# Performance work log

Measured on AMD Instinct MI355X. Metric: run time of the kernel, lower is better.

## Reference

```python
import jax, jax.numpy as jnp
import numpy as np

CHANS = [32, 32, 64, 64, 128, 128]
IN_CHANS = [1, 32, 32, 64, 64, 128]
BETA = 0.25  # VectorQuantizer_reset default; ResidualVQ's beta=0.4 is never forwarded
BN_EPS = 1e-5


def setup_inputs() -> dict:
    key = jax.random.key(0)
    ks = jax.random.split(key, 20)
    B, L, IDIM, H, NE = 64, 2000, 80, 256, 1024
    inp = {"speech": jax.random.normal(ks[0], (B, L, IDIM), jnp.float32)}
    for i, (ci, co) in enumerate(zip(IN_CHANS, CHANS)):
        inp[f"cw{i}"] = jax.random.normal(ks[1 + i], (co, ci, 3, 3), jnp.float32) * 0.05
        inp[f"g{i}"] = jnp.ones((co,), jnp.float32)
        inp[f"b{i}"] = jnp.zeros((co,), jnp.float32)
    inp["w_ih"] = jax.random.normal(ks[10], (3 * H, 256), jnp.float32) * 0.05
    inp["w_hh"] = jax.random.normal(ks[11], (3 * H, H), jnp.float32) * 0.05
    inp["bih"] = jnp.zeros((3 * H,), jnp.float32)
    inp["bhh"] = jnp.zeros((3 * H,), jnp.float32)
    for j, k in zip((1, 2, 3), (12, 13, 14)):
        inp[f"cb{j}"] = jax.random.uniform(ks[k], (NE, H), jnp.float32, -1.0 / NE, 1.0 / NE)
    return inp


def conv_bn_relu(x, w, g, b):
    # Conv2d(k=3, stride=2, pad=1, bias=False) + BatchNorm2d (training-mode batch stats) + ReLU
    y = jax.lax.conv_general_dilated(x, w, (2, 2), [(1, 1), (1, 1)],
                                     dimension_numbers=("NCHW", "OIHW", "NCHW"))
    mu = jnp.mean(y, axis=(0, 2, 3), keepdims=True)
    var = jnp.mean((y - mu) ** 2, axis=(0, 2, 3), keepdims=True)  # biased, as torch BN
    y = (y - mu) * jax.lax.rsqrt(var + BN_EPS) * g.reshape(1, -1, 1, 1) + b.reshape(1, -1, 1, 1)
    return jax.nn.relu(y)


def gru_last_hidden(x, w_ih, w_hh, bih, bhh):
    # x: (B, T, D). PyTorch GRU, 1 layer, h0 = 0; returns last hidden state (B, H).
    B = x.shape[0]
    H = w_hh.shape[1]
    xw = jnp.einsum("btd,gd->btg", x, w_ih) + bih  # (B, T, 3H), precompute input gates

    def step(h, xt):
        gh = h @ w_hh.T + bhh
        i_r, i_z, i_n = jnp.split(xt, 3, axis=-1)
        h_r, h_z, h_n = jnp.split(gh, 3, axis=-1)
        r = jax.nn.sigmoid(i_r + h_r)
        z = jax.nn.sigmoid(i_z + h_z)
        n = jnp.tanh(i_n + r * h_n)
        return (1.0 - z) * n + z * h, None

    h0 = jnp.zeros((B, H), x.dtype)
    hT, _ = jax.lax.scan(step, h0, jnp.swapaxes(xw, 0, 1))
    return hT


def vq(z, E):
    # z: (B, e_dim), E: (n_e, e_dim). Nearest-neighbor quantize + straight-through.
    d = jnp.sum(z * z, axis=1, keepdims=True) + jnp.sum(E * E, axis=1) - 2.0 * (z @ E.T)
    idx = jnp.argmin(d, axis=1)  # (B,)
    z_q = E[idx]
    loss = jnp.mean((jax.lax.stop_gradient(z_q) - z) ** 2) \
         + BETA * jnp.mean((z_q - jax.lax.stop_gradient(z)) ** 2)
    z_q_st = z + jax.lax.stop_gradient(z_q - z)
    return z_q_st, loss, idx


def reference(speech, cw0, g0, b0, cw1, g1, b1, cw2, g2, b2, cw3, g3, b3,
              cw4, g4, b4, cw5, g5, b5, w_ih, w_hh, bih, bhh, cb1, cb2, cb3):
    x = speech[:, None, :, :]  # (B, 1, L, idim)
    for w, g, b in ((cw0, g0, b0), (cw1, g1, b1), (cw2, g2, b2),
                    (cw3, g3, b3), (cw4, g4, b4), (cw5, g5, b5)):
        x = conv_bn_relu(x, w, g, b)
    B, C, T, F = x.shape
    hs = x.transpose(0, 2, 1, 3).reshape(B, T, C * F)  # (B, T', C*F)
    ref_embs = gru_last_hidden(hs, w_ih, w_hh, bih, bhh)  # (B, 256)

    residual = ref_embs
    zq1, l1, i1 = vq(residual, cb1)
    residual = residual - zq1
    zq2, l2, i2 = vq(residual, cb2)
    residual = residual - zq2
    zq3, l3, i3 = vq(residual, cb3)

    z_q_out = jnp.concatenate([zq1, zq2, zq3], axis=1)  # (B, 3*e_dim)
    vq_loss = l1 + l2 + l3
    codebooks = (zq1, zq2, zq3, zq1 + zq2 + zq3)
    return (z_q_out, vq_loss, i1[:, None], codebooks)
```

## Files before the change

### kernel.cpp

```cpp
#include <hip/hip_runtime.h>
#include <math.h>


__global__ __launch_bounds__(256) void prep_kernel(
    const float* __restrict__ w_ih, const float* __restrict__ w_hh,
    const float* __restrict__ cb0, const float* __restrict__ cb1,
    const float* __restrict__ cb2, float* __restrict__ w_ihT,
    float* __restrict__ w_hhT, float* __restrict__ ET, float* __restrict__ sE) {
  int tid = threadIdx.x;
  int y = blockIdx.y;
  if (y < 5) {
    const float* in;
    float* outp;
    int R, C;
    if (y == 0) { in = w_ih; outp = w_ihT; R = 768; C = 256; }
    else if (y == 1) { in = w_hh; outp = w_hhT; R = 768; C = 256; }
    else {
      in = (y == 2 ? cb0 : (y == 3 ? cb1 : cb2));
      outp = ET + (size_t)(y - 2) * 262144;
      R = 1024; C = 256;
    }
    int n = R * C;
    for (int t = blockIdx.x * 256 + tid; t < n; t += 64 * 256) {
      int i = t / C, j = t % C;
      outp[(size_t)j * R + i] = in[t];
    }
  } else {
    int wid = tid >> 6, lane = tid & 63;
    for (int c = blockIdx.x * 4 + wid; c < 3072; c += 64 * 4) {
      const float* E = (c < 1024 ? cb0 : (c < 2048 ? cb1 : cb2));
      int cc = c & 1023;
      float4 v4 = ((const float4*)(E + (size_t)cc * 256))[lane];
      float ssum = v4.x * v4.x + v4.y * v4.y + v4.z * v4.z + v4.w * v4.w;
#pragma unroll
      for (int m = 32; m >= 1; m >>= 1) ssum += __shfl_xor(ssum, m, 64);
      if (lane == 0) sE[c] = ssum;
    }
  }
}

__global__ __launch_bounds__(256) void conv0_stats_kernel(
    const float* __restrict__ speech, const float* __restrict__ w0,
    float* __restrict__ part) {
  constexpr int SPR = 41, SPH = 49;
  __shared__ float spE[SPH * SPR];
  __shared__ float spO[SPH * SPR];
  const int tid = threadIdx.x;
  const int bx = blockIdx.x;
  const int b = blockIdx.z;
  const int to0 = bx * 24;
  const int sr0 = 2 * to0 - 1;
  const float* sb = speech + (size_t)b * 160000;
  for (int i = tid; i < SPH * 81; i += 256) {
    int r = i / 81, c = i % 81;
    int gr = sr0 + r, gc = c - 1;
    float v = (gr >= 0 && gr < 2000 && gc >= 0 && gc < 80) ? sb[gr * 80 + gc] : 0.f;
    float* pl = (c & 1) ? spO : spE;
    pl[r * SPR + (c >> 1)] = v;
  }
  __syncthreads();

  const int fo = tid % 40;
  const int trr = tid / 40;
  const bool rowok = (trr < 6);
  const int r0 = rowok ? trr * 4 : 0;

  float xv4[4][9];
  {
    int e0 = (2 * r0) * SPR + fo;
    float p0 = spE[e0], p1 = spO[e0], p2 = spE[e0 + 1];
#pragma unroll
    for (int k = 0; k < 4; ++k) {
      int mr = (2 * (r0 + k) + 1) * SPR + fo;
      int br = mr + SPR;
      xv4[k][0] = p0; xv4[k][1] = p1; xv4[k][2] = p2;
      xv4[k][3] = spE[mr]; xv4[k][4] = spO[mr]; xv4[k][5] = spE[mr + 1];
      xv4[k][6] = spE[br]; xv4[k][7] = spO[br]; xv4[k][8] = spE[br + 1];
      p0 = xv4[k][6]; p1 = xv4[k][7]; p2 = xv4[k][8];
    }
  }
  bool val[4];
#pragma unroll
  for (int k = 0; k < 4; ++k) val[k] = rowok && (to0 + r0 + k < 1000);

  float s[32], q[32];
#pragma unroll
  for (int c = 0; c < 32; ++c) { s[c] = 0.f; q[c] = 0.f; }
#pragma unroll
  for (int c = 0; c < 32; ++c) {
    const float* wk = w0 + c * 9;
    float w0v = wk[0], w1v = wk[1], w2v = wk[2], w3v = wk[3], w4v = wk[4];
    float w5v = wk[5], w6v = wk[6], w7v = wk[7], w8v = wk[8];
#pragma unroll
    for (int k = 0; k < 4; ++k) {
      float a = xv4[k][0] * w0v;
      a = fmaf(xv4[k][1], w1v, a); a = fmaf(xv4[k][2], w2v, a);
      a = fmaf(xv4[k][3], w3v, a); a = fmaf(xv4[k][4], w4v, a);
      a = fmaf(xv4[k][5], w5v, a); a = fmaf(xv4[k][6], w6v, a);
      a = fmaf(xv4[k][7], w7v, a); a = fmaf(xv4[k][8], w8v, a);
      if (val[k]) { s[c] += a; q[c] = fmaf(a, a, q[c]); }
    }
  }
  const int wid = tid >> 6;
  const int lane = tid & 63;
  const int pidx = ((b * 42 + bx) << 2) | wid;
#pragma unroll
  for (int c = 0; c < 32; ++c) {
    float ss = s[c], qq = q[c];
#pragma unroll
    for (int m = 32; m >= 1; m >>= 1) {
      ss += __shfl_xor(ss, m, 64);
      qq += __shfl_xor(qq, m, 64);
    }
    if (lane == 0) {
      part[(size_t)c * 10752 + pidx] = ss;
      part[(size_t)(32 + c) * 10752 + pidx] = qq;
    }
  }
}

__global__ __launch_bounds__(256) void conv1_fused_kernel(
    const float* __restrict__ speech, const float* __restrict__ w0,
    const float* __restrict__ aff0, const float* __restrict__ w1,
    float* __restrict__ y, float* __restrict__ part) {
  constexpr int SPR = 41, SPH = 51;
  constexpr int LPS = 21, LTH = 25, LPL = LTH * LPS;
  __shared__ float spE[SPH * SPR];
  __shared__ float spO[SPH * SPR];
  __shared__ float l0t[2][2 * LPL];
  const int tid = threadIdx.x;
  const int bx = blockIdx.x;
  const int b = blockIdx.z;
  const int to0 = bx * 12;
  const int l0r0 = 2 * to0 - 1;
  const int sr0 = 4 * to0 - 3;
  const float* sb = speech + (size_t)b * 160000;
  for (int i = tid; i < SPH * 81; i += 256) {
    int r = i / 81, c = i % 81;
    int gr = sr0 + r, gc = c - 1;
    float v = (gr >= 0 && gr < 2000 && gc >= 0 && gc < 80) ? sb[gr * 80 + gc] : 0.f;
    float* pl = (c & 1) ? spO : spE;
    pl[r * SPR + (c >> 1)] = v;
  }

  const int fc = tid % 42;
  const int fr0 = tid / 42;
  const bool filler = (tid < 210);
  const int wcol = fc - 1;
  const bool colok = (wcol >= 0) && (wcol < 40);
  const int wc = colok ? wcol : 0;
  const int r0 = fr0 * 5;
  const int lplane = (fc & 1) * LPL;
  const int lidx = fc >> 1;

  const int fo = tid % 20;
  const int tr = tid / 20;
  const int to = to0 + tr;
  const bool active = (tr < 12) && (to < 500);
  const int trc = (tr < 12) ? tr : 0;

  float acc[32];
#pragma unroll
  for (int c = 0; c < 32; ++c) acc[c] = 0.f;

  __syncthreads();

#define L0FILL(CIDX, BF)                                                      \
  if (filler) {                                                               \
    const float* wk = w0 + (CIDX) * 9;                                        \
    const float wv0 = wk[0], wv1 = wk[1], wv2 = wk[2], wv3 = wk[3];           \
    const float wv4 = wk[4], wv5 = wk[5], wv6 = wk[6], wv7 = wk[7];           \
    const float wv8 = wk[8];                                                  \
    const float sc = aff0[CIDX], sh = aff0[32 + (CIDX)];                      \
    int e0 = (2 * r0) * SPR + wc;                                             \
    float t0 = spE[e0], t1 = spO[e0], t2 = spE[e0 + 1];                       \
    _Pragma("unroll")                                                         \
    for (int k = 0; k < 5; ++k) {                                             \
      int r = r0 + k;                                                         \
      int mr = (2 * r + 1) * SPR + wc;                                        \
      int br = mr + SPR;                                                      \
      float m0 = spE[mr], m1 = spO[mr], m2 = spE[mr + 1];                     \
      float b0 = spE[br], b1 = spO[br], b2 = spE[br + 1];                     \
      float a = t0 * wv0;                                                     \
      a = fmaf(t1, wv1, a); a = fmaf(t2, wv2, a);                             \
      a = fmaf(m0, wv3, a); a = fmaf(m1, wv4, a); a = fmaf(m2, wv5, a);       \
      a = fmaf(b0, wv6, a); a = fmaf(b1, wv7, a); a = fmaf(b2, wv8, a);       \
      int h0 = l0r0 + r;                                                      \
      bool ok = colok && h0 >= 0 && h0 < 1000;                                \
      float vv = ok ? fmaxf(fmaf(a, sc, sh), 0.f) : 0.f;                      \
      l0t[BF][lplane + r * LPS + lidx] = vv;                                  \
      t0 = b0; t1 = b1; t2 = b2;                                              \
    }                                                                         \
  }

  L0FILL(0, 0)
  __syncthreads();

  for (int ci = 0; ci < 32; ++ci) {
    int cur = ci & 1;
    if (ci + 1 < 32) { L0FILL(ci + 1, cur ^ 1) }
    float xv[9];
    const int rb = 2 * trc;
#pragma unroll
    for (int t = 0; t < 9; ++t) {
      int dr = t / 3, m = t % 3;
      xv[t] = l0t[cur][(m == 1 ? LPL : 0) + (rb + dr) * LPS + fo + (m == 2 ? 1 : 0)];
    }
    const float* wp = w1 + ci * 9;
#pragma unroll
    for (int c = 0; c < 32; ++c) {
      const float* wcp = wp + (size_t)c * 32 * 9;
#pragma unroll
      for (int t = 0; t < 9; ++t) acc[c] = fmaf(xv[t], wcp[t], acc[c]);
    }
    __syncthreads();
  }
#undef L0FILL

  if (active) {
#pragma unroll
    for (int c = 0; c < 32; ++c)
      y[(((size_t)b * 32 + c) * 500 + to) * 20 + fo] = acc[c];
  }

  const int wid = tid >> 6;
  const int lane = tid & 63;
  const int pidx = ((b * 42 + bx) << 2) | wid;
#pragma unroll
  for (int c = 0; c < 32; ++c) {
    float v = active ? acc[c] : 0.f;
    float qq = v * v;
#pragma unroll
    for (int m = 32; m >= 1; m >>= 1) {
      v += __shfl_xor(v, m, 64);
      qq += __shfl_xor(qq, m, 64);
    }
    if (lane == 0) {
      part[(size_t)c * 10752 + pidx] = v;
      part[(size_t)(32 + c) * 10752 + pidx] = qq;
    }
  }
}

template <int CI, int COG, int WO, int ROWS, int WI, int HI, int HO>
__global__ __launch_bounds__(256) void conv_kernel(
    const float* __restrict__ x, const float* __restrict__ w,
    const float* __restrict__ aff, float* __restrict__ y, int CO,
    float* __restrict__ part) {
  constexpr int TW = WI + 2;
  constexpr int PE = (TW + 1) / 2;
  constexpr int PS = PE | 1;
  constexpr int TH = 2 * ROWS + 1;
  constexpr int PL = TH * PS;
  constexpr int TN = TH * TW;
  constexpr int F = (TN + 255) / 256;
  __shared__ float tile[2][2 * PL];

  const int tid = threadIdx.x;
  const int fo = tid % WO;
  const int tr = tid / WO;
  const int to0 = blockIdx.x * ROWS;
  const int to = to0 + tr;
  const int co0 = blockIdx.y * COG;
  const int b = blockIdx.z;
  const bool active = (tr < ROWS) && (to < HO);
  const int trc = (tr < ROWS) ? tr : 0;

  int fa[F], fof[F];
  bool fv[F], fw[F];
#pragma unroll
  for (int j = 0; j < F; ++j) {
    int i = tid + j * 256;
    int r = i / TW, c = i % TW;
    int gih = 2 * to0 - 1 + r;
    int giw = c - 1;
    bool inb = (i < TN);
    bool v = inb && gih >= 0 && gih < HI && giw >= 0 && giw < WI;
    fw[j] = inb;
    fv[j] = v;
    fof[j] = v ? (gih * WI + giw) : 0;
    fa[j] = inb ? ((c & 1) * PL + r * PS + (c >> 1)) : 0;
  }

  float acc[COG];
#pragma unroll
  for (int c = 0; c < COG; ++c) acc[c] = 0.f;

  const float* xb = x + (size_t)b * CI * HI * WI;

  {
    const float sc = aff[0], sh = aff[CI];
#pragma unroll
    for (int j = 0; j < F; ++j) {
      if (fw[j]) {
        float v = xb[fof[j]];
        v = fv[j] ? fmaxf(fmaf(v, sc, sh), 0.f) : 0.f;
        tile[0][fa[j]] = v;
      }
    }
  }
  __syncthreads();

  for (int ci = 0; ci < CI; ++ci) {
    int cur = ci & 1;
    if (ci + 1 < CI) {
      const float* xc = xb + (size_t)(ci + 1) * HI * WI;
      const float sc = aff[ci + 1], sh = aff[CI + ci + 1];
#pragma unroll
      for (int j = 0; j < F; ++j) {
        if (fw[j]) {
          float v = xc[fof[j]];
          v = fv[j] ? fmaxf(fmaf(v, sc, sh), 0.f) : 0.f;
          tile[cur ^ 1][fa[j]] = v;
        }
      }
    }
    float xv[9];
    const int rb = 2 * trc;
#pragma unroll
    for (int t = 0; t < 9; ++t) {
      int dr = t / 3, m = t % 3;
      xv[t] = tile[cur][(m == 1 ? PL : 0) + (rb + dr) * PS + fo + (m == 2 ? 1 : 0)];
    }
    const float* wp = w + ((size_t)co0 * CI + ci) * 9;
#pragma unroll
    for (int c = 0; c < COG; ++c) {
      const float* wc = wp + (size_t)c * CI * 9;
#pragma unroll
      for (int t = 0; t < 9; ++t) acc[c] = fmaf(xv[t], wc[t], acc[c]);
    }
    __syncthreads();
  }

  if (active) {
#pragma unroll
    for (int c = 0; c < COG; ++c)
      y[(((size_t)b * CO + co0 + c) * HO + to) * WO + fo] = acc[c];
  }

  const int wid = tid >> 6;
  const int lane = tid & 63;
  const int P = (int)(gridDim.z * gridDim.x) * 4;
  const int pidx = ((b * (int)gridDim.x + (int)blockIdx.x) << 2) | wid;
#pragma unroll
  for (int c = 0; c < COG; ++c) {
    float v = active ? acc[c] : 0.f;
    float qq = v * v;
#pragma unroll
    for (int m = 32; m >= 1; m >>= 1) {
      v += __shfl_xor(v, m, 64);
      qq += __shfl_xor(qq, m, 64);
    }
    if (lane == 0) {
      part[(size_t)(co0 + c) * P + pidx] = v;
      part[(size_t)(CO + co0 + c) * P + pidx] = qq;
    }
  }
}

__global__ __launch_bounds__(256) void conv5_kernel(
    const float* __restrict__ x, const float* __restrict__ w5,
    const float* __restrict__ aff, float* __restrict__ part5) {
  constexpr int TW = 5, PS = 3, TH = 65, PL = TH * PS, TN = TH * TW;
  __shared__ float tile[2][2 * PL];
  const int tid = threadIdx.x;
  const int p = tid & 63;
  const int to = p >> 1, fo = p & 1;
  const int cog = tid >> 6;
  const int co0 = cog * 32;
  const int ci0 = blockIdx.y * 32;
  const int b = blockIdx.z;

  int fa[2], fof[2];
  bool fv[2], fw[2];
#pragma unroll
  for (int j = 0; j < 2; ++j) {
    int i = tid + j * 256;
    int r = i / TW, c = i % TW;
    int gih = r - 1, giw = c - 1;
    bool inb = (i < TN);
    bool v = inb && gih >= 0 && gih < 63 && giw >= 0 && giw < 3;
    fw[j] = inb;
    fv[j] = v;
    fof[j] = v ? (gih * 3 + giw) : 0;
    fa[j] = inb ? ((c & 1) * PL + r * PS + (c >> 1)) : 0;
  }

  float acc[32];
#pragma unroll
  for (int c = 0; c < 32; ++c) acc[c] = 0.f;

  const float* xb = x + (size_t)b * 128 * 189;

  {
    const float sc = aff[ci0], sh = aff[128 + ci0];
    const float* xc = xb + (size_t)ci0 * 189;
#pragma unroll
    for (int j = 0; j < 2; ++j) {
      if (fw[j]) {
        float v = xc[fof[j]];
        v = fv[j] ? fmaxf(fmaf(v, sc, sh), 0.f) : 0.f;
        tile[0][fa[j]] = v;
      }
    }
  }
  __syncthreads();

  for (int cc = 0; cc < 32; ++cc) {
    int cur = cc & 1;
    int ci = ci0 + cc;
    if (cc + 1 < 32) {
      const float* xc = xb + (size_t)(ci + 1) * 189;
      const float sc = aff[ci + 1], sh = aff[128 + ci + 1];
#pragma unroll
      for (int j = 0; j < 2; ++j) {
        if (fw[j]) {
          float v = xc[fof[j]];
          v = fv[j] ? fmaxf(fmaf(v, sc, sh), 0.f) : 0.f;
          tile[cur ^ 1][fa[j]] = v;
        }
      }
    }
    float xv[9];
#pragma unroll
    for (int t = 0; t < 9; ++t) {
      int dr = t / 3, m = t % 3;
      xv[t] = tile[cur][(m == 1 ? PL : 0) + (2 * to + dr) * PS + fo + (m == 2 ? 1 : 0)];
    }
    const float* wp = w5 + ((size_t)co0 * 128 + ci) * 9;
#pragma unroll
    for (int c = 0; c < 32; ++c) {
      const float* wc = wp + (size_t)c * 128 * 9;
#pragma unroll
      for (int t = 0; t < 9; ++t) acc[c] = fmaf(xv[t], wc[t], acc[c]);
    }
    __syncthreads();
  }

#pragma unroll
  for (int c = 0; c < 32; ++c)
    part5[(((size_t)blockIdx.y * 64 + b) * 128 + co0 + c) * 64 + p] = acc[c];
}

__global__ __launch_bounds__(256) void reduce4st_kernel(const float* __restrict__ p,
                                                        float* __restrict__ y,
                                                        float* __restrict__ part) {
  int i = blockIdx.x * 256 + threadIdx.x;
  float s = p[i] + p[i + 524288] + p[i + 2 * 524288] + p[i + 3 * 524288];
  y[i] = s;
  float q = s * s;
  float ss = s;
#pragma unroll
  for (int m = 32; m >= 1; m >>= 1) {
    ss += __shfl_xor(ss, m, 64);
    q += __shfl_xor(q, m, 64);
  }
  if ((threadIdx.x & 63) == 0) {
    int c = (i >> 6) & 127;
    int b = i >> 13;
    part[(size_t)c * 64 + b] = ss;
    part[(size_t)(128 + c) * 64 + b] = q;
  }
}

__global__ __launch_bounds__(256) void bn_finalize(
    const float* __restrict__ part, const float* __restrict__ g,
    const float* __restrict__ bb, float* __restrict__ aff, int CO, int P,
    double invN) {
  __shared__ double s1[256];
  __shared__ double s2[256];
  int c = blockIdx.x, tid = threadIdx.x;
  double a = 0, q = 0;
  for (int i = tid; i < P; i += 256) {
    a += (double)part[(size_t)c * P + i];
    q += (double)part[(size_t)(CO + c) * P + i];
  }
  s1[tid] = a;
  s2[tid] = q;
  __syncthreads();
  for (int s = 128; s > 0; s >>= 1) {
    if (tid < s) { s1[tid] += s1[tid + s]; s2[tid] += s2[tid + s]; }
    __syncthreads();
  }
  if (tid == 0) {
    double mean = s1[0] * invN;
    double var = s2[0] * invN - mean * mean;
    float scale = g[c] * (float)(1.0 / sqrt(var + 1e-5));
    aff[c] = scale;
    aff[CO + c] = bb[c] - (float)mean * scale;
  }
}

__global__ __launch_bounds__(256) void xw_kernel(const float* __restrict__ act5,
                                                 const float* __restrict__ aff5,
                                                 const float* __restrict__ w_ihT,
                                                 const float* __restrict__ bih,
                                                 float* __restrict__ xw) {
  __shared__ float sh[8 * 256];
  int tid = threadIdx.x;
  int bt0 = blockIdx.x * 8;
  int b = bt0 >> 5;
  for (int i = tid; i < 2048; i += 256) {
    int r = i >> 8, d = i & 255, c = d >> 1, f = d & 1;
    int t = (bt0 + r) & 31;
    float v = act5[(((size_t)b * 128 + c) * 32 + t) * 2 + f];
    sh[i] = fmaxf(fmaf(v, aff5[c], aff5[128 + c]), 0.f);
  }
  __syncthreads();
  float acc[3][8];
#pragma unroll
  for (int g = 0; g < 3; ++g)
#pragma unroll
    for (int r = 0; r < 8; ++r) acc[g][r] = 0.f;
  for (int k = 0; k < 256; ++k) {
    float w0 = w_ihT[k * 768 + tid];
    float w1 = w_ihT[k * 768 + 256 + tid];
    float w2 = w_ihT[k * 768 + 512 + tid];
#pragma unroll
    for (int r = 0; r < 8; ++r) {
      float hv = sh[r * 256 + k];
      acc[0][r] = fmaf(hv, w0, acc[0][r]);
      acc[1][r] = fmaf(hv, w1, acc[1][r]);
      acc[2][r] = fmaf(hv, w2, acc[2][r]);
    }
  }
  float b0 = bih[tid], b1 = bih[256 + tid], b2 = bih[512 + tid];
  for (int r = 0; r < 8; ++r) {
    size_t base = (size_t)(bt0 + r) * 768;
    xw[base + tid] = acc[0][r] + b0;
    xw[base + 256 + tid] = acc[1][r] + b1;
    xw[base + 512 + tid] = acc[2][r] + b2;
  }
}

__global__ __launch_bounds__(768) void gru_kernel(const float* __restrict__ xw,
                                                  const float* __restrict__ w_hhT,
                                                  const float* __restrict__ bhh,
                                                  float* __restrict__ zout) {
  __shared__ __align__(16) float h[256];
  __shared__ float gh[768];
  int b = blockIdx.x, j = threadIdx.x;
  if (j < 256) h[j] = 0.f;
  __syncthreads();
  float bh = bhh[j];
  for (int t = 0; t < 32; ++t) {
    float acc = 0.f;
    const float4* h4 = (const float4*)h;
#pragma unroll 8
    for (int k4 = 0; k4 < 64; ++k4) {
      float4 hv = h4[k4];
      const float* wr = w_hhT + (4 * k4) * 768 + j;
      acc = fmaf(hv.x, wr[0], acc);
      acc = fmaf(hv.y, wr[768], acc);
      acc = fmaf(hv.z, wr[1536], acc);
      acc = fmaf(hv.w, wr[2304], acc);
    }
    gh[j] = acc + bh;
    __syncthreads();
    if (j < 256) {
      const float* xt = xw + ((size_t)b * 32 + t) * 768;
      float ir = xt[j], iz = xt[256 + j], inn = xt[512 + j];
      float r = 1.f / (1.f + expf(-(ir + gh[j])));
      float zz = 1.f / (1.f + expf(-(iz + gh[256 + j])));
      float n = tanhf(fmaf(r, gh[512 + j], inn));
      h[j] = (1.f - zz) * n + zz * h[j];
    }
    __syncthreads();
  }
  if (j < 256) zout[(size_t)b * 256 + j] = h[j];
}

__global__ __launch_bounds__(256) void vq_all_kernel(
    const float* __restrict__ zb, const float* __restrict__ ET,
    const float* __restrict__ sE, const float* __restrict__ cb0,
    const float* __restrict__ cb1, const float* __restrict__ cb2,
    float* __restrict__ out, float* __restrict__ msep) {
  const size_t OFF_I1 = 49153;
  const size_t OFF_CB = 49217;
  const size_t OFF_CBSUM = 98369;
  __shared__ float rz[256];
  __shared__ float rs[256];
  __shared__ int ri[256];
  int b = blockIdx.x, tid = threadIdx.x;
  float z0 = zb[(size_t)b * 256 + tid];
  rz[tid] = z0;
  float zqs = 0.f;
  for (int s = 0; s < 3; ++s) {
    __syncthreads();
    const float* ETs = ET + (size_t)s * 262144;
    const float* sEs = sE + s * 1024;
    const float* E = (s == 0 ? cb0 : (s == 1 ? cb1 : cb2));
    float a0 = 0.f, a1 = 0.f, a2 = 0.f, a3 = 0.f;
    for (int k = 0; k < 256; ++k) {
      float zk = rz[k];
      const float* row = ETs + (size_t)k * 1024 + tid;
      a0 = fmaf(zk, row[0], a0);
      a1 = fmaf(zk, row[256], a1);
      a2 = fmaf(zk, row[512], a2);
      a3 = fmaf(zk, row[768], a3);
    }
    float s0 = sEs[tid] - 2.f * a0;
    float s1 = sEs[256 + tid] - 2.f * a1;
    float s2 = sEs[512 + tid] - 2.f * a2;
    float s3 = sEs[768 + tid] - 2.f * a3;
    float bs = s0;
    int bi = tid;
    if (s1 < bs) { bs = s1; bi = 256 + tid; }
    if (s2 < bs) { bs = s2; bi = 512 + tid; }
    if (s3 < bs) { bs = s3; bi = 768 + tid; }
    rs[tid] = bs;
    ri[tid] = bi;
    __syncthreads();
    for (int st = 128; st > 0; st >>= 1) {
      if (tid < st) {
        float os = rs[tid + st];
        int oi = ri[tid + st];
        if (os < rs[tid] || (os == rs[tid] && oi < ri[tid])) {
          rs[tid] = os;
          ri[tid] = oi;
        }
      }
      __syncthreads();
    }
    int idx = ri[0];
    if (s == 0 && tid == 0) out[OFF_I1 + b] = (float)idx;
    float zq = E[(size_t)idx * 256 + tid];
    float rv = rz[tid];
    float d = zq - rv;
    out[(size_t)b * 768 + s * 256 + tid] = zq;
    out[OFF_CB + (size_t)s * 16384 + (size_t)b * 256 + tid] = zq;
    zqs += zq;
    rz[tid] = rv - zq;
    rs[tid] = d * d;
    __syncthreads();
    for (int st = 128; st > 0; st >>= 1) {
      if (tid < st) rs[tid] += rs[tid + st];
      __syncthreads();
    }
    if (tid == 0) msep[s * 64 + b] = rs[0];
  }
  out[OFF_CBSUM + (size_t)b * 256 + tid] = zqs;
}

__global__ void loss_kernel(const float* __restrict__ msep, float* __restrict__ out) {
  if (threadIdx.x == 0 && blockIdx.x == 0) {
    float s = 0.f;
    for (int i = 0; i < 192; ++i) s += msep[i];
    out[0] = 1.25f * s / 16384.0f;
  }
}

extern "C" void kernel_launch(void* const* d_in, const int* in_sizes, int n_in,
                              void* d_out, int out_size, void* d_ws, size_t ws_size,
                              hipStream_t stream) {
  const float* speech = (const float*)d_in[0];
  const float* cw[6];
  const float* gg[6];
  const float* bbp[6];
  for (int i = 0; i < 6; ++i) {
    cw[i] = (const float*)d_in[1 + 3 * i];
    gg[i] = (const float*)d_in[2 + 3 * i];
    bbp[i] = (const float*)d_in[3 + 3 * i];
  }
  const float* w_ih = (const float*)d_in[19];
  const float* w_hh = (const float*)d_in[20];
  const float* bih = (const float*)d_in[21];
  const float* bhh = (const float*)d_in[22];
  const float* cb[3] = {(const float*)d_in[23], (const float*)d_in[24], (const float*)d_in[25]};
  float* out = (float*)d_out;
  float* ws_f = (float*)d_ws;
  (void)in_sizes; (void)n_in; (void)out_size;

  size_t off = 0;
  float* act1 = ws_f + off; off += 20480000ull;
  float* act2 = ws_f + off; off += 10240000ull;
  float* act3 = ws_f + off; off += 2560000ull;
  float* part = ws_f + off; off += 700000ull;
  float* affs = ws_f + off; off += 1536ull;
  float* w_ihT = ws_f + off; off += 196608ull;
  float* w_hhT = ws_f + off; off += 196608ull;
  float* xw = ws_f + off; off += 1572864ull;
  float* zb = ws_f + off; off += 16384ull;
  float* ET = ws_f + off; off += 786432ull;
  float* sEp = ws_f + off; off += 3072ull;
  float* msep = ws_f + off; off += 192ull;

  if (ws_size < off * sizeof(float)) return;

  float* part5 = act1;
  float* act4 = act2;
  float* act5 = act3;

  const size_t OFF_LOSS = 49152;

  prep_kernel<<<dim3(64, 6), 256, 0, stream>>>(w_ih, w_hh, cb[0], cb[1], cb[2],
                                               w_ihT, w_hhT, ET, sEp);

  conv0_stats_kernel<<<dim3(42, 1, 64), 256, 0, stream>>>(speech, cw[0], part);
  bn_finalize<<<32, 256, 0, stream>>>(part, gg[0], bbp[0], affs + 0, 32, 10752,
                                      1.0 / 2560000.0);
  conv1_fused_kernel<<<dim3(42, 1, 64), 256, 0, stream>>>(speech, cw[0], affs + 0,
                                                          cw[1], act1, part);
  bn_finalize<<<32, 256, 0, stream>>>(part, gg[1], bbp[1], affs + 256, 32, 10752,
                                      1.0 / 640000.0);
  conv_kernel<32, 32, 10, 25, 20, 500, 250>
      <<<dim3(10, 2, 64), 256, 0, stream>>>(act1, cw[2], affs + 256, act2, 64, part);
  bn_finalize<<<64, 256, 0, stream>>>(part, gg[2], bbp[2], affs + 512, 64, 2560,
                                      1.0 / 160000.0);
  conv_kernel<64, 16, 5, 42, 10, 250, 125>
      <<<dim3(3, 4, 64), 256, 0, stream>>>(act2, cw[3], affs + 512, act3, 64, part);
  bn_finalize<<<64, 256, 0, stream>>>(part, gg[3], bbp[3], affs + 768, 64, 768,
                                      1.0 / 40000.0);
  conv_kernel<64, 16, 3, 63, 5, 125, 63>
      <<<dim3(1, 8, 64), 256, 0, stream>>>(act3, cw[4], affs + 768, act4, 128, part);
  bn_finalize<<<128, 256, 0, stream>>>(part, gg[4], bbp[4], affs + 1024, 128, 256,
                                       1.0 / 12096.0);
  conv5_kernel<<<dim3(1, 4, 64), 256, 0, stream>>>(act4, cw[5], affs + 1024, part5);
  reduce4st_kernel<<<2048, 256, 0, stream>>>(part5, act5, part);
  bn_finalize<<<128, 256, 0, stream>>>(part, gg[5], bbp[5], affs + 1280, 128, 64,
                                       1.0 / 4096.0);

  xw_kernel<<<256, 256, 0, stream>>>(act5, affs + 1280, w_ihT, bih, xw);
  gru_kernel<<<64, 768, 0, stream>>>(xw, w_hhT, bhh, zb);

  vq_all_kernel<<<64, 256, 0, stream>>>(zb, ET, sEp, cb[0], cb[1], cb[2], out, msep);
  loss_kernel<<<1, 64, 0, stream>>>(msep, out + OFF_LOSS);
}
```

Before: 1.199 ms.

## Split conv1 and conv5 across more blocks and shorten conv0 stat reductions

Conv1's fused kernel now splits its 32 output channels across two blocks in the y dimension. Each block keeps 16 accumulators, which lowers register pressure and doubles the grid, at the cost of recomputing the layer-0 input tile in both blocks. Conv5 splits its input channels into 8 groups instead of 4, and an 8-way partial-sum reducer replaces the 4-way one. Conv0's stats kernel stops its shuffle reduction at 4 lanes and writes 4x more partials (into act1) for bn_finalize to sum, saving shuffle steps but adding reduction work downstream.

```diff
diff --git a/kernel.cpp b/kernel.cpp
--- a/kernel.cpp
+++ b/kernel.cpp
@@ -103,18 +103,18 @@
   }
   const int wid = tid >> 6;
   const int lane = tid & 63;
-  const int pidx = ((b * 42 + bx) << 2) | wid;
+  const int pidx = (((b * 42 + bx) << 2) | wid) << 2;
 #pragma unroll
   for (int c = 0; c < 32; ++c) {
     float ss = s[c], qq = q[c];
 #pragma unroll
-    for (int m = 32; m >= 1; m >>= 1) {
+    for (int m = 32; m >= 4; m >>= 1) {
       ss += __shfl_xor(ss, m, 64);
       qq += __shfl_xor(qq, m, 64);
     }
-    if (lane == 0) {
-      part[(size_t)c * 10752 + pidx] = ss;
-      part[(size_t)(32 + c) * 10752 + pidx] = qq;
+    if (lane < 4) {
+      part[(size_t)c * 43008 + pidx + lane] = ss;
+      part[(size_t)(32 + c) * 43008 + pidx + lane] = qq;
     }
   }
 }
@@ -130,6 +130,7 @@
   __shared__ float l0t[2][2 * LPL];
   const int tid = threadIdx.x;
   const int bx = blockIdx.x;
+  const int co0 = blockIdx.y * 16;
   const int b = blockIdx.z;
   const int to0 = bx * 12;
   const int l0r0 = 2 * to0 - 1;
@@ -159,9 +160,9 @@
   const bool active = (tr < 12) && (to < 500);
   const int trc = (tr < 12) ? tr : 0;
 
-  float acc[32];
-#pragma unroll
-  for (int c = 0; c < 32; ++c) acc[c] = 0.f;
+  float acc[16];
+#pragma unroll
+  for (int c = 0; c < 16; ++c) acc[c] = 0.f;
 
   __syncthreads();
 
@@ -206,9 +207,9 @@
       int dr = t / 3, m = t % 3;
       xv[t] = l0t[cur][(m == 1 ? LPL : 0) + (rb + dr) * LPS + fo + (m == 2 ? 1 : 0)];
     }
-    const float* wp = w1 + ci * 9;
-#pragma unroll
-    for (int c = 0; c < 32; ++c) {
+    const float* wp = w1 + ((size_t)co0 * 32 + ci) * 9;
+#pragma unroll
+    for (int c = 0; c < 16; ++c) {
       const float* wcp = wp + (size_t)c * 32 * 9;
 #pragma unroll
       for (int t = 0; t < 9; ++t) acc[c] = fmaf(xv[t], wcp[t], acc[c]);
@@ -219,15 +220,15 @@
 
   if (active) {
 #pragma unroll
-    for (int c = 0; c < 32; ++c)
-      y[(((size_t)b * 32 + c) * 500 + to) * 20 + fo] = acc[c];
+    for (int c = 0; c < 16; ++c)
+      y[(((size_t)b * 32 + co0 + c) * 500 + to) * 20 + fo] = acc[c];
   }
 
   const int wid = tid >> 6;
   const int lane = tid & 63;
   const int pidx = ((b * 42 + bx) << 2) | wid;
 #pragma unroll
-  for (int c = 0; c < 32; ++c) {
+  for (int c = 0; c < 16; ++c) {
     float v = active ? acc[c] : 0.f;
     float qq = v * v;
 #pragma unroll
@@ -236,8 +237,8 @@
       qq += __shfl_xor(qq, m, 64);
     }
     if (lane == 0) {
-      part[(size_t)c * 10752 + pidx] = v;
-      part[(size_t)(32 + c) * 10752 + pidx] = qq;
+      part[(size_t)(co0 + c) * 10752 + pidx] = v;
+      part[(size_t)(32 + co0 + c) * 10752 + pidx] = qq;
     }
   }
 }
@@ -368,7 +369,7 @@
   const int to = p >> 1, fo = p & 1;
   const int cog = tid >> 6;
   const int co0 = cog * 32;
-  const int ci0 = blockIdx.y * 32;
+  const int ci0 = blockIdx.y * 16;
   const int b = blockIdx.z;
 
   int fa[2], fof[2];
@@ -406,10 +407,10 @@
   }
   __syncthreads();
 
-  for (int cc = 0; cc < 32; ++cc) {
+  for (int cc = 0; cc < 16; ++cc) {
     int cur = cc & 1;
     int ci = ci0 + cc;
-    if (cc + 1 < 32) {
+    if (cc + 1 < 16) {
       const float* xc = xb + (size_t)(ci + 1) * 189;
       const float sc = aff[ci + 1], sh = aff[128 + ci + 1];
 #pragma unroll
@@ -442,11 +443,13 @@
     part5[(((size_t)blockIdx.y * 64 + b) * 128 + co0 + c) * 64 + p] = acc[c];
 }
 
-__global__ __launch_bounds__(256) void reduce4st_kernel(const float* __restrict__ p,
+__global__ __launch_bounds__(256) void reduce8st_kernel(const float* __restrict__ p,
                                                         float* __restrict__ y,
                                                         float* __restrict__ part) {
   int i = blockIdx.x * 256 + threadIdx.x;
-  float s = p[i] + p[i + 524288] + p[i + 2 * 524288] + p[i + 3 * 524288];
+  float s = 0.f;
+#pragma unroll
+  for (int k = 0; k < 8; ++k) s += p[i + (size_t)k * 524288];
   y[i] = s;
   float q = s * s;
   float ss = s;
@@ -687,6 +690,7 @@
 
   if (ws_size < off * sizeof(float)) return;
 
+  float* part0 = act1;
   float* part5 = act1;
   float* act4 = act2;
   float* act5 = act3;
@@ -696,10 +700,10 @@
   prep_kernel<<<dim3(64, 6), 256, 0, stream>>>(w_ih, w_hh, cb[0], cb[1], cb[2],
                                                w_ihT, w_hhT, ET, sEp);
 
-  conv0_stats_kernel<<<dim3(42, 1, 64), 256, 0, stream>>>(speech, cw[0], part);
-  bn_finalize<<<32, 256, 0, stream>>>(part, gg[0], bbp[0], affs + 0, 32, 10752,
+  conv0_stats_kernel<<<dim3(42, 1, 64), 256, 0, stream>>>(speech, cw[0], part0);
+  bn_finalize<<<32, 256, 0, stream>>>(part0, gg[0], bbp[0], affs + 0, 32, 43008,
                                       1.0 / 2560000.0);
-  conv1_fused_kernel<<<dim3(42, 1, 64), 256, 0, stream>>>(speech, cw[0], affs + 0,
+  conv1_fused_kernel<<<dim3(42, 2, 64), 256, 0, stream>>>(speech, cw[0], affs + 0,
                                                           cw[1], act1, part);
   bn_finalize<<<32, 256, 0, stream>>>(part, gg[1], bbp[1], affs + 256, 32, 10752,
                                       1.0 / 640000.0);
@@ -715,8 +719,8 @@
       <<<dim3(1, 8, 64), 256, 0, stream>>>(act3, cw[4], affs + 768, act4, 128, part);
   bn_finalize<<<128, 256, 0, stream>>>(part, gg[4], bbp[4], affs + 1024, 128, 256,
                                        1.0 / 12096.0);
-  conv5_kernel<<<dim3(1, 4, 64), 256, 0, stream>>>(act4, cw[5], affs + 1024, part5);
-  reduce4st_kernel<<<2048, 256, 0, stream>>>(part5, act5, part);
+  conv5_kernel<<<dim3(1, 8, 64), 256, 0, stream>>>(act4, cw[5], affs + 1024, part5);
+  reduce8st_kernel<<<2048, 256, 0, stream>>>(part5, act5, part);
   bn_finalize<<<128, 256, 0, stream>>>(part, gg[5], bbp[5], affs + 1280, 128, 64,
                                        1.0 / 4096.0);
 
```

Measured after the change: 1.707 ms. 1.42x slower.
